# Optimization experiments

Measured on AMD Instinct MI355X. Metric: run time of the kernel, lower is better.

The kernel has to match this reference:

```python
import jax, jax.numpy as jnp
import numpy as np

N, E, G, T, H, ED, IN_D, OUT_D = 50000, 1600000, 64, 5, 64, 9, 10, 3
EPS = 1e-6

def _seg_mean(vals, seg, num):
    s = jax.ops.segment_sum(vals, seg, num_segments=num)
    c = jax.ops.segment_sum(jnp.ones((vals.shape[0],), vals.dtype), seg, num_segments=num)
    return s / jnp.maximum(c, 1.0)[:, None], c

def per_graph_edge_norm(edge_attr, edge_graph, num_graphs):
    # standardize each edge-feature column per graph (zero-shot transfer trick)
    mu, _ = _seg_mean(edge_attr, edge_graph, num_graphs)
    sq, _ = _seg_mean(edge_attr * edge_attr, edge_graph, num_graphs)
    var = jnp.maximum(sq - mu * mu, 0.0)
    std = jnp.sqrt(var)
    return (edge_attr - mu[edge_graph]) / (std[edge_graph] + EPS)

def setup_inputs() -> dict:
    key = jax.random.key(0)
    ks = jax.random.split(key, 24)
    s = 0.05  # weight scale to keep ReLU chains stable
    inp = {
        'x': jax.random.normal(ks[0], (N, IN_D), jnp.float32),
        'edge_index': jax.random.randint(ks[1], (2, E), 0, N),
        'edge_attr': jax.random.normal(ks[2], (E, ED), jnp.float32),
        'batch': jnp.sort(jax.random.randint(ks[3], (N,), 0, G)),
        'lift_W1': jax.random.normal(ks[4], (IN_D, H), jnp.float32) * s,
        'lift_b1': jnp.zeros((H,), jnp.float32),
        'lift_W2': jax.random.normal(ks[5], (H, H), jnp.float32) * s,
        'lift_b2': jnp.zeros((H,), jnp.float32),
        'Wself': jax.random.normal(ks[6], (T, H, H), jnp.float32) * s,
        'bself': jnp.zeros((T, H), jnp.float32),
        'msg_W0': jax.random.normal(ks[7], (T, H + ED, H), jnp.float32) * s,
        'msg_b0': jnp.zeros((T, H), jnp.float32),
        'msg_W1': jax.random.normal(ks[8], (T, H, H), jnp.float32) * s,
        'msg_b1': jnp.zeros((T, H), jnp.float32),
        'msg_W2': jax.random.normal(ks[9], (T, H, H), jnp.float32) * s,
        'msg_b2': jnp.zeros((T, H), jnp.float32),
        'gate_W': jax.random.normal(ks[10], (T, 1, H), jnp.float32) * s,
        'gate_b': jnp.zeros((T, H), jnp.float32),
        'proj_W1': jax.random.normal(ks[11], (H, H), jnp.float32) * s,
        'proj_b1': jnp.zeros((H,), jnp.float32),
        'proj_W2': jax.random.normal(ks[12], (H, OUT_D), jnp.float32) * s,
        'proj_b2': jnp.zeros((OUT_D,), jnp.float32),
    }
    return inp

def _gno(x, edge_index, edge_attr, batch,
         lift_W1, lift_b1, lift_W2, lift_b2,
         Wself, bself, msg_W0, msg_b0, msg_W1, msg_b1, msg_W2, msg_b2,
         gate_W, gate_b, proj_W1, proj_b1, proj_W2, proj_b2):
    src, dst = edge_index[0], edge_index[1]
    edge_graph = batch[src]
    ea = per_graph_edge_norm(edge_attr, edge_graph, G)  # cols 0:9 == all cols
    log_diag_y = x[:, 4:5]                               # [N,1]
    v0 = jax.nn.relu(x @ lift_W1 + lift_b1) @ lift_W2 + lift_b2  # lift
    v = v0
    for t in range(T):
        # gather -> per-edge MLP -> scatter-mean (AdmittanceKernelLayer)
        h = jnp.concatenate([v[src], ea], axis=-1)              # [E, H+ED]
        h = jax.nn.relu(h @ msg_W0[t] + msg_b0[t])
        h = jax.nn.relu(h @ msg_W1[t] + msg_b1[t])
        m = h @ msg_W2[t] + msg_b2[t]                           # [E, H]
        agg, _ = _seg_mean(m, dst, N)                           # mean aggregation
        gate = jax.nn.sigmoid(log_diag_y @ gate_W[t] + gate_b[t])  # [N,H]
        v = jax.nn.relu(v @ Wself[t] + bself[t] + agg + v0) * gate
        # dropout inactive at inference
    out = jax.nn.relu(v @ proj_W1 + proj_b1) @ proj_W2 + proj_b2  # project
    return out

def reference(x, edge_index, edge_attr, batch,
              lift_W1, lift_b1, lift_W2, lift_b2,
              Wself, bself, msg_W0, msg_b0, msg_W1, msg_b1, msg_W2, msg_b2,
              gate_W, gate_b, proj_W1, proj_b1, proj_W2, proj_b2):
    return _gno(x, edge_index, edge_attr, batch,
                lift_W1, lift_b1, lift_W2, lift_b2,
                Wself, bself, msg_W0, msg_b0, msg_W1, msg_b1, msg_W2, msg_b2,
                gate_W, gate_b, proj_W1, proj_b1, proj_W2, proj_b2)
```

## Files before the change

kernel.cpp:

```cpp
#include <hip/hip_runtime.h>
#include <math.h>

#define NN 50000
#define NE 1600000
#define NG 64
#define NT 5
#define NH 64
#define NED 9
#define NIN 10
#define NOUT 3
#define EPSF 1e-6f
#define NSUB (NE / 16)

typedef __attribute__((ext_vector_type(8))) short s8v;
typedef __attribute__((ext_vector_type(4))) short s4v;
typedef __attribute__((ext_vector_type(4))) float f32x4;

__device__ __forceinline__ unsigned short f2bf(float f) {
    union { float f; unsigned int u; } v; v.f = f;
    unsigned int r = v.u + 0x7FFFu + ((v.u >> 16) & 1u);
    return (unsigned short)(r >> 16);
}
__device__ __forceinline__ float bf2f(unsigned short b) {
    union { unsigned int u; float f; } v; v.u = ((unsigned int)b) << 16;
    return v.f;
}

__global__ void stats_kernel(const int* __restrict__ ei, const float* __restrict__ ea,
                             const int* __restrict__ batch,
                             float* __restrict__ ssum, float* __restrict__ ssq,
                             float* __restrict__ scnt, int* __restrict__ ecnt) {
    __shared__ float lsum[NG * NED];
    __shared__ float lsq[NG * NED];
    __shared__ float lcnt[NG];
    for (int i = threadIdx.x; i < NG * NED; i += blockDim.x) { lsum[i] = 0.f; lsq[i] = 0.f; }
    for (int i = threadIdx.x; i < NG; i += blockDim.x) lcnt[i] = 0.f;
    __syncthreads();
    int lane = threadIdx.x & 63;
    int stride = gridDim.x * blockDim.x;
    for (int e = blockIdx.x * blockDim.x + threadIdx.x; e < NE; e += stride) {
        int s = ei[e];
        int g = batch[s];
        atomicAdd(&ecnt[ei[NE + e]], 1);
        float a[NED];
#pragma unroll
        for (int d = 0; d < NED; ++d) a[d] = ea[(size_t)e * NED + d];
        int g0 = __builtin_amdgcn_readfirstlane(g);
        if (__all(g == g0)) {
            float sv[NED], qv[NED];
#pragma unroll
            for (int d = 0; d < NED; ++d) { sv[d] = a[d]; qv[d] = a[d] * a[d]; }
#pragma unroll
            for (int off = 32; off; off >>= 1) {
#pragma unroll
                for (int d = 0; d < NED; ++d) {
                    sv[d] += __shfl_down(sv[d], off);
                    qv[d] += __shfl_down(qv[d], off);
                }
            }
            if (lane == 0) {
#pragma unroll
                for (int d = 0; d < NED; ++d) {
                    atomicAdd(&lsum[g0 * NED + d], sv[d]);
                    atomicAdd(&lsq[g0 * NED + d], qv[d]);
                }
                atomicAdd(&lcnt[g0], 64.f);
            }
        } else {
            atomicAdd(&lcnt[g], 1.0f);
#pragma unroll
            for (int d = 0; d < NED; ++d) {
                atomicAdd(&lsum[g * NED + d], a[d]);
                atomicAdd(&lsq[g * NED + d], a[d] * a[d]);
            }
        }
    }
    __syncthreads();
    for (int i = threadIdx.x; i < NG * NED; i += blockDim.x) {
        atomicAdd(&ssum[i], lsum[i]);
        atomicAdd(&ssq[i], lsq[i]);
    }
    for (int i = threadIdx.x; i < NG; i += blockDim.x) atomicAdd(&scnt[i], lcnt[i]);
}

__global__ void stats_fin(const float* __restrict__ ssum, const float* __restrict__ ssq,
                          const float* __restrict__ scnt,
                          float* __restrict__ mu, float* __restrict__ rstd) {
    int i = blockIdx.x * blockDim.x + threadIdx.x;
    if (i >= NG * NED) return;
    int g = i / NED;
    float c = fmaxf(scnt[g], 1.0f);
    float m = ssum[i] / c;
    float q = ssq[i] / c;
    float var = fmaxf(q - m * m, 0.f);
    mu[i] = m;
    rstd[i] = 1.0f / (sqrtf(var) + EPSF);
}

__global__ void scan1_kernel(const int* __restrict__ ecnt, int* __restrict__ partial) {
    __shared__ int sm[256];
    int i = blockIdx.x * 256 + threadIdx.x;
    sm[threadIdx.x] = (i < NN) ? ecnt[i] : 0;
    __syncthreads();
    for (int off = 128; off; off >>= 1) {
        if (threadIdx.x < off) sm[threadIdx.x] += sm[threadIdx.x + off];
        __syncthreads();
    }
    if (threadIdx.x == 0) partial[blockIdx.x] = sm[0];
}
__global__ void scan2_kernel(int* __restrict__ partial, int nb) {
    __shared__ int sm[256];
    int t = threadIdx.x;
    sm[t] = (t < nb) ? partial[t] : 0;
    __syncthreads();
    for (int off = 1; off < 256; off <<= 1) {
        int v = (t >= off) ? sm[t - off] : 0;
        __syncthreads();
        sm[t] += v;
        __syncthreads();
    }
    if (t < nb) partial[t] = (t ? sm[t - 1] : 0);
}
__global__ void scan3_kernel(const int* __restrict__ ecnt, const int* __restrict__ partial,
                             int* __restrict__ offs) {
    __shared__ int sm[256];
    int b = blockIdx.x, t = threadIdx.x, i = b * 256 + t;
    int x = (i < NN) ? ecnt[i] : 0;
    sm[t] = x;
    __syncthreads();
    for (int off = 1; off < 256; off <<= 1) {
        int v = (t >= off) ? sm[t - off] : 0;
        __syncthreads();
        sm[t] += v;
        __syncthreads();
    }
    if (i < NN) offs[i] = sm[t] - x + partial[b];
}

__global__ void permute_kernel(const int* __restrict__ ei, const int* __restrict__ offs,
                               int* __restrict__ cursor, int* __restrict__ perm) {
    int stride = gridDim.x * blockDim.x;
    for (int e = blockIdx.x * blockDim.x + threadIdx.x; e < NE; e += stride) {
        int d = ei[NE + e];
        int pos = offs[d] + atomicAdd(&cursor[d], 1);
        perm[pos] = e;
    }
}

__global__ void pack_kernel(const int* __restrict__ perm, const int* __restrict__ ei,
                            const float* __restrict__ ea, const int* __restrict__ batch,
                            const float* __restrict__ mu, const float* __restrict__ rstd,
                            int* __restrict__ srcPerm, int* __restrict__ dstPerm,
                            unsigned short* __restrict__ eaN) {
    int stride = gridDim.x * blockDim.x;
    for (int p = blockIdx.x * blockDim.x + threadIdx.x; p < NE; p += stride) {
        int e = perm[p];
        int s = ei[e], d = ei[NE + e];
        int g = batch[s];
        srcPerm[p] = s;
        dstPerm[p] = d;
#pragma unroll
        for (int k = 0; k < NED; ++k) {
            float val = (ea[(size_t)e * NED + k] - mu[g * NED + k]) * rstd[g * NED + k];
            eaN[(size_t)k * NE + p] = f2bf(val);
        }
    }
}

__global__ __launch_bounds__(256) void lift_kernel(
    const float* __restrict__ x,
    const float* __restrict__ W1, const float* __restrict__ b1,
    const float* __restrict__ W2, const float* __restrict__ b2,
    float* __restrict__ v0, float* __restrict__ v, float* __restrict__ ldy) {
    __shared__ float sW1[NIN * NH];
    __shared__ __align__(16) float sW2[NH][NH];
    __shared__ float sb1[NH], sb2[NH];
    for (int i = threadIdx.x; i < NIN * NH; i += blockDim.x) sW1[i] = W1[i];
    for (int i = threadIdx.x; i < NH * NH; i += blockDim.x) {
        int k = i >> 6, j = i & 63;
        sW2[j][k] = W2[i];
    }
    for (int i = threadIdx.x; i < NH; i += blockDim.x) { sb1[i] = b1[i]; sb2[i] = b2[i]; }
    __syncthreads();
    int stride = gridDim.x * blockDim.x;
    for (int n = blockIdx.x * blockDim.x + threadIdx.x; n < NN; n += stride) {
        float xr[NIN];
#pragma unroll
        for (int k = 0; k < NIN; ++k) xr[k] = x[(size_t)n * NIN + k];
        ldy[n] = xr[4];
        float h[NH];
#pragma unroll
        for (int j = 0; j < NH; ++j) {
            float acc = sb1[j];
#pragma unroll
            for (int k = 0; k < NIN; ++k) acc += xr[k] * sW1[k * NH + j];
            h[j] = fmaxf(acc, 0.f);
        }
#pragma unroll
        for (int j = 0; j < NH; ++j) {
            float acc = sb2[j];
#pragma unroll
            for (int k = 0; k < NH; k += 4) {
                float4 w = *(const float4*)&sW2[j][k];
                acc += h[k] * w.x + h[k + 1] * w.y + h[k + 2] * w.z + h[k + 3] * w.w;
            }
            v0[(size_t)n * NH + j] = acc;
            v[(size_t)n * NH + j] = acc;
        }
    }
}

__device__ __forceinline__ void gemm_acc68(const float* __restrict__ Ab,
                                           const float* __restrict__ Wb,
                                           int K, int te, int tj, float acc[4][4]) {
#pragma unroll 4
    for (int k = 0; k < K; ++k) {
        float4 a = *(const float4*)(Ab + k * 68 + (te << 2));
        float4 b = *(const float4*)(Wb + (k << 6) + (tj << 2));
        acc[0][0] = fmaf(a.x, b.x, acc[0][0]);
        acc[0][1] = fmaf(a.x, b.y, acc[0][1]);
        acc[0][2] = fmaf(a.x, b.z, acc[0][2]);
        acc[0][3] = fmaf(a.x, b.w, acc[0][3]);
        acc[1][0] = fmaf(a.y, b.x, acc[1][0]);
        acc[1][1] = fmaf(a.y, b.y, acc[1][1]);
        acc[1][2] = fmaf(a.y, b.z, acc[1][2]);
        acc[1][3] = fmaf(a.y, b.w, acc[1][3]);
        acc[2][0] = fmaf(a.z, b.x, acc[2][0]);
        acc[2][1] = fmaf(a.z, b.y, acc[2][1]);
        acc[2][2] = fmaf(a.z, b.z, acc[2][2]);
        acc[2][3] = fmaf(a.z, b.w, acc[2][3]);
        acc[3][0] = fmaf(a.w, b.x, acc[3][0]);
        acc[3][1] = fmaf(a.w, b.y, acc[3][1]);
        acc[3][2] = fmaf(a.w, b.z, acc[3][2]);
        acc[3][3] = fmaf(a.w, b.w, acc[3][3]);
    }
}

__global__ __launch_bounds__(256, 4) void u_kernel(
    const float* __restrict__ v, const float* __restrict__ W0v,
    const float* __restrict__ b0, float* __restrict__ U) {
    __shared__ __align__(16) float Vt[64][68];
    __shared__ __align__(16) float sW[64][64];
    __shared__ float sb[64];
    const int tid = threadIdx.x;
    const int base = blockIdx.x * 64;
    const int te = tid >> 4, tj = tid & 15;

    {
        int r = tid >> 2;
        int kb = (tid & 3) << 4;
        int n = base + r;
        const float4* vrow = (const float4*)(v + (size_t)n * NH + kb);
#pragma unroll
        for (int q = 0; q < 4; ++q) {
            float4 f = (n < NN) ? vrow[q] : make_float4(0.f, 0.f, 0.f, 0.f);
            int k = kb + q * 4;
            Vt[k + 0][r] = f.x; Vt[k + 1][r] = f.y; Vt[k + 2][r] = f.z; Vt[k + 3][r] = f.w;
        }
    }
    for (int i4 = tid; i4 < 64 * 16; i4 += 256) {
        int k = i4 >> 4, c4 = i4 & 15;
        *(float4*)&sW[k][c4 * 4] = *(const float4*)(W0v + (size_t)k * 64 + c4 * 4);
    }
    if (tid < 64) sb[tid] = b0[tid];
    __syncthreads();

    float acc[4][4];
    {
        float b0_ = sb[tj * 4 + 0], b1_ = sb[tj * 4 + 1], b2_ = sb[tj * 4 + 2], b3_ = sb[tj * 4 + 3];
#pragma unroll
        for (int ee = 0; ee < 4; ++ee) { acc[ee][0] = b0_; acc[ee][1] = b1_; acc[ee][2] = b2_; acc[ee][3] = b3_; }
    }
    gemm_acc68(&Vt[0][0], &sW[0][0], 64, te, tj, acc);

#pragma unroll
    for (int ee = 0; ee < 4; ++ee) {
        int n = base + te * 4 + ee;
        if (n < NN)
            *(float4*)&U[(size_t)n * NH + tj * 4] =
                make_float4(acc[ee][0], acc[ee][1], acc[ee][2], acc[ee][3]);
    }
}

__global__ __launch_bounds__(256, 4) void edge4_kernel(
    const int* __restrict__ srcPerm, const int* __restrict__ dstPerm,
    const unsigned short* __restrict__ eaN,
    const float* __restrict__ W0e, const float* __restrict__ W1, const float* __restrict__ b1,
    const float* __restrict__ U, float* __restrict__ nodesum) {
    __shared__ __align__(16) float sWe[NED][64];
    __shared__ __align__(16) short W1frag[8][64][8];
    __shared__ __align__(16) short h0bf[4][16 * 64];
    __shared__ __align__(16) float h1s[4][16 * 64];
    __shared__ int sDstS[4][16];

    const int tid = threadIdx.x;
    const int lane = tid & 63, w = tid >> 6;
    const int l15 = lane & 15, l4 = lane >> 4;

    for (int i4 = tid; i4 < NED * 16; i4 += 256) {
        int k = i4 >> 4, c4 = i4 & 15;
        *(float4*)&sWe[k][c4 * 4] = *(const float4*)(W0e + (size_t)k * 64 + c4 * 4);
    }
    for (int idx = tid; idx < 2 * 4 * 64; idx += 256) {
        int kc = idx >> 8, c = (idx >> 6) & 3, ln = idx & 63;
        int fl15 = ln & 15, fl4 = ln >> 4;
        int col = 16 * c + fl15;
        s8v frag;
#pragma unroll
        for (int j = 0; j < 8; ++j) {
            int k = kc * 32 + fl4 * 8 + j;
            frag[j] = (short)f2bf(W1[(size_t)k * 64 + col]);
        }
        *(s8v*)&W1frag[kc * 4 + c][ln][0] = frag;
    }
    float b1r[4];
#pragma unroll
    for (int c = 0; c < 4; ++c) b1r[c] = b1[16 * c + l15];
    __syncthreads();

    short* myh0 = h0bf[w];
    float* myh1 = h1s[w];
    int*   myd  = sDstS[w];
    const int gw = blockIdx.x * 4 + w;
    const int nw = gridDim.x * 4;

    for (int st = gw; st < NSUB; st += nw) {
        const int e16 = st * 16;
        if (lane < 16) myd[lane] = dstPerm[e16 + lane];

        int4 s4 = *(const int4*)(srcPerm + e16 + 4 * l4);
        ushort4 eu[NED];
#pragma unroll
        for (int d = 0; d < NED; ++d)
            eu[d] = *(const ushort4*)(eaN + (size_t)d * NE + e16 + 4 * l4);

        float acc0[4][4];
        {
            const int* sp = (const int*)&s4;
#pragma unroll
            for (int ee = 0; ee < 4; ++ee) {
                float4 u4 = *(const float4*)(U + (size_t)sp[ee] * NH + 4 * l15);
                acc0[ee][0] = u4.x; acc0[ee][1] = u4.y; acc0[ee][2] = u4.z; acc0[ee][3] = u4.w;
            }
        }
#pragma unroll
        for (int d = 0; d < NED; ++d) {
            float4 wv = *(const float4*)&sWe[d][4 * l15];
            float a0 = bf2f(eu[d].x), a1 = bf2f(eu[d].y), a2 = bf2f(eu[d].z), a3 = bf2f(eu[d].w);
            acc0[0][0] = fmaf(a0, wv.x, acc0[0][0]); acc0[0][1] = fmaf(a0, wv.y, acc0[0][1]);
            acc0[0][2] = fmaf(a0, wv.z, acc0[0][2]); acc0[0][3] = fmaf(a0, wv.w, acc0[0][3]);
            acc0[1][0] = fmaf(a1, wv.x, acc0[1][0]); acc0[1][1] = fmaf(a1, wv.y, acc0[1][1]);
            acc0[1][2] = fmaf(a1, wv.z, acc0[1][2]); acc0[1][3] = fmaf(a1, wv.w, acc0[1][3]);
            acc0[2][0] = fmaf(a2, wv.x, acc0[2][0]); acc0[2][1] = fmaf(a2, wv.y, acc0[2][1]);
            acc0[2][2] = fmaf(a2, wv.z, acc0[2][2]); acc0[2][3] = fmaf(a2, wv.w, acc0[2][3]);
            acc0[3][0] = fmaf(a3, wv.x, acc0[3][0]); acc0[3][1] = fmaf(a3, wv.y, acc0[3][1]);
            acc0[3][2] = fmaf(a3, wv.z, acc0[3][2]); acc0[3][3] = fmaf(a3, wv.w, acc0[3][3]);
        }

#pragma unroll
        for (int ee = 0; ee < 4; ++ee) {
            int row = 4 * l4 + ee;
            s4v p;
            p[0] = (short)f2bf(fmaxf(acc0[ee][0], 0.f));
            p[1] = (short)f2bf(fmaxf(acc0[ee][1], 0.f));
            p[2] = (short)f2bf(fmaxf(acc0[ee][2], 0.f));
            p[3] = (short)f2bf(fmaxf(acc0[ee][3], 0.f));
            *(s4v*)((char*)myh0 + row * 128 + ((l15 * 8) ^ ((row & 7) << 4))) = p;
        }

        f32x4 acc[4];
#pragma unroll
        for (int c = 0; c < 4; ++c) {
            float b = b1r[c];
            acc[c][0] = b; acc[c][1] = b; acc[c][2] = b; acc[c][3] = b;
        }
        {
            const char* abase = (const char*)myh0 + l15 * 128;
            const int aswz = (l15 & 7) << 4;
#pragma unroll
            for (int kc = 0; kc < 2; ++kc) {
                s8v af = *(const s8v*)(abase + ((l4 * 16 + kc * 64) ^ aswz));
#pragma unroll
                for (int c = 0; c < 4; ++c) {
                    s8v bf = *(const s8v*)&W1frag[kc * 4 + c][lane][0];
                    acc[c] = __builtin_amdgcn_mfma_f32_16x16x32_bf16(af, bf, acc[c], 0, 0, 0);
                }
            }
        }

        int dFirst = myd[0];
        int dLast = myd[15];
        if (dFirst == dLast) {
#pragma unroll
            for (int c = 0; c < 4; ++c) {
                float vs = fmaxf(acc[c][0], 0.f) + fmaxf(acc[c][1], 0.f) +
                           fmaxf(acc[c][2], 0.f) + fmaxf(acc[c][3], 0.f);
                vs += __shfl_xor(vs, 16);
                vs += __shfl_xor(vs, 32);
                if (l4 == 0)
                    atomicAdd(&nodesum[(size_t)dFirst * NH + 16 * c + l15], vs);
            }
        } else {
#pragma unroll
            for (int r = 0; r < 4; ++r) {
                int row = 4 * l4 + r;
#pragma unroll
                for (int c = 0; c < 4; ++c)
                    myh1[row * 64 + ((16 * c + l15) ^ (l4 * 8))] = fmaxf(acc[c][r], 0.f);
            }
            int cur = dFirst;
            float a = myh1[lane];
#pragma unroll
            for (int i = 1; i < 16; ++i) {
                int dn = myd[i];
                float hv = myh1[i * 64 + (lane ^ ((i >> 2) * 8))];
                if (dn != cur) {
                    atomicAdd(&nodesum[(size_t)cur * NH + lane], a);
                    cur = dn;
                    a = hv;
                } else {
                    a += hv;
                }
            }
            atomicAdd(&nodesum[(size_t)cur * NH + lane], a);
        }
    }
}

__global__ __launch_bounds__(256, 2) void update3_kernel(
    const float* __restrict__ Wself, const float* __restrict__ bself,
    const float* __restrict__ W2, const float* __restrict__ b2,
    const float* __restrict__ gWt, const float* __restrict__ gbt,
    const float* __restrict__ v0, const float* __restrict__ ldy,
    const int* __restrict__ ecnt, const float* __restrict__ nodesum,
    float* __restrict__ v) {
    __shared__ __align__(16) float Vt[64][68];
    __shared__ __align__(16) float St[64][68];
    __shared__ __align__(16) float sWs[64][64];
    __shared__ __align__(16) float sW2[64][64];
    __shared__ float sbs[64], sb2[64], sgw[64], sgb[64];
    const int tid = threadIdx.x;
    const int base = blockIdx.x * 64;
    const int te = tid >> 4, tj = tid & 15;

    {
        int r = tid >> 2;
        int kb = (tid & 3) << 4;
        int n = base + r;
        const float4* vrow = (const float4*)(v + (size_t)n * NH + kb);
        const float4* srow = (const float4*)(nodesum + (size_t)n * NH + kb);
#pragma unroll
        for (int q = 0; q < 4; ++q) {
            float4 f = (n < NN) ? vrow[q] : make_float4(0.f, 0.f, 0.f, 0.f);
            float4 g = (n < NN) ? srow[q] : make_float4(0.f, 0.f, 0.f, 0.f);
            int k = kb + q * 4;
            Vt[k + 0][r] = f.x; Vt[k + 1][r] = f.y; Vt[k + 2][r] = f.z; Vt[k + 3][r] = f.w;
            St[k + 0][r] = g.x; St[k + 1][r] = g.y; St[k + 2][r] = g.z; St[k + 3][r] = g.w;
        }
    }
    for (int i4 = tid; i4 < 64 * 16; i4 += 256) {
        int k = i4 >> 4, c4 = i4 & 15;
        *(float4*)&sWs[k][c4 * 4] = *(const float4*)(Wself + (size_t)k * 64 + c4 * 4);
        *(float4*)&sW2[k][c4 * 4] = *(const float4*)(W2 + (size_t)k * 64 + c4 * 4);
    }
    if (tid < 64) { sbs[tid] = bself[tid]; sb2[tid] = b2[tid]; sgw[tid] = gWt[tid]; sgb[tid] = gbt[tid]; }
    __syncthreads();

    float acc1[4][4], acc2[4][4];
    {
        float b0_ = sbs[tj * 4 + 0], b1_ = sbs[tj * 4 + 1], b2_ = sbs[tj * 4 + 2], b3_ = sbs[tj * 4 + 3];
#pragma unroll
        for (int ee = 0; ee < 4; ++ee) {
            acc1[ee][0] = b0_; acc1[ee][1] = b1_; acc1[ee][2] = b2_; acc1[ee][3] = b3_;
            acc2[ee][0] = 0.f; acc2[ee][1] = 0.f; acc2[ee][2] = 0.f; acc2[ee][3] = 0.f;
        }
    }
    gemm_acc68(&Vt[0][0], &sWs[0][0], 64, te, tj, acc1);
    gemm_acc68(&St[0][0], &sW2[0][0], 64, te, tj, acc2);

    float gw0 = sgw[tj * 4 + 0], gw1 = sgw[tj * 4 + 1], gw2 = sgw[tj * 4 + 2], gw3 = sgw[tj * 4 + 3];
    float gb0 = sgb[tj * 4 + 0], gb1 = sgb[tj * 4 + 1], gb2 = sgb[tj * 4 + 2], gb3 = sgb[tj * 4 + 3];
    float bb0 = sb2[tj * 4 + 0], bb1 = sb2[tj * 4 + 1], bb2 = sb2[tj * 4 + 2], bb3 = sb2[tj * 4 + 3];
#pragma unroll
    for (int ee = 0; ee < 4; ++ee) {
        int n = base + te * 4 + ee;
        if (n >= NN) continue;
        float cnt = (float)ecnt[n];
        float has = (cnt > 0.5f) ? 1.f : 0.f;
        float dninv = has / fmaxf(cnt, 1.f);
        float ld = ldy[n];
        float4 v0r = *(const float4*)&v0[(size_t)n * NH + tj * 4];
        float z0 = acc1[ee][0] + acc2[ee][0] * dninv + bb0 * has + v0r.x;
        float z1 = acc1[ee][1] + acc2[ee][1] * dninv + bb1 * has + v0r.y;
        float z2 = acc1[ee][2] + acc2[ee][2] * dninv + bb2 * has + v0r.z;
        float z3 = acc1[ee][3] + acc2[ee][3] * dninv + bb3 * has + v0r.w;
        float g0 = 1.f / (1.f + expf(-(ld * gw0 + gb0)));
        float g1 = 1.f / (1.f + expf(-(ld * gw1 + gb1)));
        float g2 = 1.f / (1.f + expf(-(ld * gw2 + gb2)));
        float g3 = 1.f / (1.f + expf(-(ld * gw3 + gb3)));
        *(float4*)&v[(size_t)n * NH + tj * 4] =
            make_float4(fmaxf(z0, 0.f) * g0, fmaxf(z1, 0.f) * g1,
                        fmaxf(z2, 0.f) * g2, fmaxf(z3, 0.f) * g3);
    }
}

__global__ __launch_bounds__(256) void proj_kernel(
    const float* __restrict__ v,
    const float* __restrict__ pW1, const float* __restrict__ pb1,
    const float* __restrict__ pW2, const float* __restrict__ pb2,
    float* __restrict__ out) {
    __shared__ __align__(16) float sW1[NH][NH];
    __shared__ float sb1[NH];
    __shared__ float sW2[NH * NOUT];
    __shared__ float sb2[NOUT];
    for (int i = threadIdx.x; i < NH * NH; i += blockDim.x) {
        int k = i >> 6, j = i & 63;
        sW1[j][k] = pW1[i];
    }
    for (int i = threadIdx.x; i < NH; i += blockDim.x) sb1[i] = pb1[i];
    for (int i = threadIdx.x; i < NH * NOUT; i += blockDim.x) sW2[i] = pW2[i];
    for (int i = threadIdx.x; i < NOUT; i += blockDim.x) sb2[i] = pb2[i];
    __syncthreads();
    int stride = gridDim.x * blockDim.x;
    for (int n = blockIdx.x * blockDim.x + threadIdx.x; n < NN; n += stride) {
        float vr[NH];
        const float4* vp = (const float4*)(v + (size_t)n * NH);
#pragma unroll
        for (int q = 0; q < NH / 4; ++q) {
            float4 f = vp[q];
            vr[4 * q + 0] = f.x; vr[4 * q + 1] = f.y; vr[4 * q + 2] = f.z; vr[4 * q + 3] = f.w;
        }
        float o0 = sb2[0], o1 = sb2[1], o2 = sb2[2];
#pragma unroll
        for (int j = 0; j < NH; ++j) {
            float acc = sb1[j];
#pragma unroll
            for (int k = 0; k < NH; k += 4) {
                float4 w = *(const float4*)&sW1[j][k];
                acc += vr[k] * w.x + vr[k + 1] * w.y + vr[k + 2] * w.z + vr[k + 3] * w.w;
            }
            float h = fmaxf(acc, 0.f);
            o0 += h * sW2[j * NOUT + 0];
            o1 += h * sW2[j * NOUT + 1];
            o2 += h * sW2[j * NOUT + 2];
        }
        out[(size_t)n * NOUT + 0] = o0;
        out[(size_t)n * NOUT + 1] = o1;
        out[(size_t)n * NOUT + 2] = o2;
    }
}

extern "C" void kernel_launch(void* const* d_in, const int* in_sizes, int n_in,
                              void* d_out, int out_size, void* d_ws, size_t ws_size,
                              hipStream_t stream) {
    (void)in_sizes; (void)n_in; (void)out_size; (void)ws_size;
    const float* x     = (const float*)d_in[0];
    const int*   ei    = (const int*)d_in[1];
    const float* ea    = (const float*)d_in[2];
    const int*   batch = (const int*)d_in[3];
    const float* lW1   = (const float*)d_in[4];
    const float* lb1   = (const float*)d_in[5];
    const float* lW2   = (const float*)d_in[6];
    const float* lb2   = (const float*)d_in[7];
    const float* Wself = (const float*)d_in[8];
    const float* bself = (const float*)d_in[9];
    const float* mW0   = (const float*)d_in[10];
    const float* mb0   = (const float*)d_in[11];
    const float* mW1   = (const float*)d_in[12];
    const float* mb1   = (const float*)d_in[13];
    const float* mW2   = (const float*)d_in[14];
    const float* mb2   = (const float*)d_in[15];
    const float* gW    = (const float*)d_in[16];
    const float* gb    = (const float*)d_in[17];
    const float* pW1   = (const float*)d_in[18];
    const float* pb1   = (const float*)d_in[19];
    const float* pW2   = (const float*)d_in[20];
    const float* pb2   = (const float*)d_in[21];
    float* out = (float*)d_out;
    float* ws  = (float*)d_ws;

    float* nodesum = ws;
    float* v0   = nodesum + (size_t)NN * NH;
    float* v    = v0 + (size_t)NN * NH;
    float* U    = v + (size_t)NN * NH;
    float* ldy  = U + (size_t)NN * NH;
    float* mu   = ldy + NN;
    float* rstd = mu + NG * NED;
    float* ssum = rstd + NG * NED;
    float* ssq  = ssum + NG * NED;
    float* scnt = ssq + NG * NED;
    int*   ecnt   = (int*)(scnt + NG);
    int*   cursor = ecnt + NN;
    int*   offs    = cursor + NN;
    int*   partial = offs + NN;
    int*   srcPerm = partial + 256;
    int*   dstPerm = srcPerm + NE;
    unsigned short* eaN = (unsigned short*)(dstPerm + NE);
    int*   perm = (int*)nodesum;

    const int NBLK = (NN + 63) / 64;
    const int SBLK = (NN + 255) / 256;

    hipMemsetAsync(ssum, 0, ((size_t)(2 * NG * NED + NG) + 2 * NN) * sizeof(float), stream);

    stats_kernel<<<512, 256, 0, stream>>>(ei, ea, batch, ssum, ssq, scnt, ecnt);
    stats_fin<<<3, 256, 0, stream>>>(ssum, ssq, scnt, mu, rstd);
    scan1_kernel<<<SBLK, 256, 0, stream>>>(ecnt, partial);
    scan2_kernel<<<1, 256, 0, stream>>>(partial, SBLK);
    scan3_kernel<<<SBLK, 256, 0, stream>>>(ecnt, partial, offs);
    permute_kernel<<<2048, 256, 0, stream>>>(ei, offs, cursor, perm);
    pack_kernel<<<2048, 256, 0, stream>>>(perm, ei, ea, batch, mu, rstd, srcPerm, dstPerm, eaN);
    lift_kernel<<<200, 256, 0, stream>>>(x, lW1, lb1, lW2, lb2, v0, v, ldy);

    for (int t = 0; t < NT; ++t) {
        const float* W0t = mW0 + (size_t)t * (NH + NED) * NH;
        hipMemsetAsync(nodesum, 0, (size_t)NN * NH * sizeof(float), stream);
        u_kernel<<<NBLK, 256, 0, stream>>>(v, W0t, mb0 + (size_t)t * NH, U);
        edge4_kernel<<<1024, 256, 0, stream>>>(
            srcPerm, dstPerm, eaN,
            W0t + (size_t)NH * NH,
            mW1 + (size_t)t * NH * NH, mb1 + (size_t)t * NH,
            U, nodesum);
        update3_kernel<<<NBLK, 256, 0, stream>>>(
            Wself + (size_t)t * NH * NH, bself + (size_t)t * NH,
            mW2 + (size_t)t * NH * NH, mb2 + (size_t)t * NH,
            gW + (size_t)t * NH, gb + (size_t)t * NH,
            v0, ldy, ecnt, nodesum, v);
    }
    proj_kernel<<<200, 256, 0, stream>>>(v, pW1, pb1, pW2, pb2, out);
}
```

Baseline: 1.366 ms.

## Replace global stats atomics with per-block partials and fold nodesum zeroing into update

The stats kernel now writes each block's shared-memory partial sums to a private slice, and a separate merge kernel reduces them deterministically, removing global float atomics and the wavefront-uniform shuffle fast path. The update kernel zeroes nodesum after reading it, so the per-iteration memset is replaced by a single memset before the loop. This saves four full 12.8MB memsets, at the cost of an extra store per element in update, a serial 1024-iteration merge loop, and simpler per-lane LDS atomics in stats.

Result: slower. 1.432 ms (+4.8%).

```diff
diff --git a/kernel.cpp b/kernel.cpp
--- a/kernel.cpp
+++ b/kernel.cpp
@@ -11,6 +11,8 @@
 #define NOUT 3
 #define EPSF 1e-6f
 #define NSUB (NE / 16)
+#define STATS_BLKS 1024
+#define STATS_SLICE (2 * NG * NED + NG)
 
 typedef __attribute__((ext_vector_type(8))) short s8v;
 typedef __attribute__((ext_vector_type(4))) short s4v;
@@ -26,61 +28,48 @@
     return v.f;
 }
 
-__global__ void stats_kernel(const int* __restrict__ ei, const float* __restrict__ ea,
-                             const int* __restrict__ batch,
-                             float* __restrict__ ssum, float* __restrict__ ssq,
-                             float* __restrict__ scnt, int* __restrict__ ecnt) {
+__global__ __launch_bounds__(256) void stats_kernel(
+    const int* __restrict__ ei, const float* __restrict__ ea,
+    const int* __restrict__ batch,
+    float* __restrict__ blockAcc, int* __restrict__ ecnt) {
     __shared__ float lsum[NG * NED];
     __shared__ float lsq[NG * NED];
     __shared__ float lcnt[NG];
     for (int i = threadIdx.x; i < NG * NED; i += blockDim.x) { lsum[i] = 0.f; lsq[i] = 0.f; }
     for (int i = threadIdx.x; i < NG; i += blockDim.x) lcnt[i] = 0.f;
     __syncthreads();
-    int lane = threadIdx.x & 63;
     int stride = gridDim.x * blockDim.x;
     for (int e = blockIdx.x * blockDim.x + threadIdx.x; e < NE; e += stride) {
         int s = ei[e];
         int g = batch[s];
         atomicAdd(&ecnt[ei[NE + e]], 1);
-        float a[NED];
-#pragma unroll
-        for (int d = 0; d < NED; ++d) a[d] = ea[(size_t)e * NED + d];
-        int g0 = __builtin_amdgcn_readfirstlane(g);
-        if (__all(g == g0)) {
-            float sv[NED], qv[NED];
-#pragma unroll
-            for (int d = 0; d < NED; ++d) { sv[d] = a[d]; qv[d] = a[d] * a[d]; }
-#pragma unroll
-            for (int off = 32; off; off >>= 1) {
-#pragma unroll
-                for (int d = 0; d < NED; ++d) {
-                    sv[d] += __shfl_down(sv[d], off);
-                    qv[d] += __shfl_down(qv[d], off);
-                }
-            }
-            if (lane == 0) {
-#pragma unroll
-                for (int d = 0; d < NED; ++d) {
-                    atomicAdd(&lsum[g0 * NED + d], sv[d]);
-                    atomicAdd(&lsq[g0 * NED + d], qv[d]);
-                }
-                atomicAdd(&lcnt[g0], 64.f);
-            }
-        } else {
-            atomicAdd(&lcnt[g], 1.0f);
-#pragma unroll
-            for (int d = 0; d < NED; ++d) {
-                atomicAdd(&lsum[g * NED + d], a[d]);
-                atomicAdd(&lsq[g * NED + d], a[d] * a[d]);
-            }
-        }
-    }
-    __syncthreads();
+        atomicAdd(&lcnt[g], 1.0f);
+#pragma unroll
+        for (int d = 0; d < NED; ++d) {
+            float a = ea[(size_t)e * NED + d];
+            atomicAdd(&lsum[g * NED + d], a);
+            atomicAdd(&lsq[g * NED + d], a * a);
+        }
+    }
+    __syncthreads();
+    float* dst = blockAcc + (size_t)blockIdx.x * STATS_SLICE;
     for (int i = threadIdx.x; i < NG * NED; i += blockDim.x) {
-        atomicAdd(&ssum[i], lsum[i]);
-        atomicAdd(&ssq[i], lsq[i]);
-    }
-    for (int i = threadIdx.x; i < NG; i += blockDim.x) atomicAdd(&scnt[i], lcnt[i]);
+        dst[i] = lsum[i];
+        dst[NG * NED + i] = lsq[i];
+    }
+    for (int i = threadIdx.x; i < NG; i += blockDim.x) dst[2 * NG * NED + i] = lcnt[i];
+}
+
+__global__ void stats_merge(const float* __restrict__ blockAcc,
+                            float* __restrict__ ssum, float* __restrict__ ssq,
+                            float* __restrict__ scnt) {
+    int i = blockIdx.x * 256 + threadIdx.x;
+    if (i >= STATS_SLICE) return;
+    float a = 0.f;
+    for (int b = 0; b < STATS_BLKS; ++b) a += blockAcc[(size_t)b * STATS_SLICE + i];
+    if (i < NG * NED) ssum[i] = a;
+    else if (i < 2 * NG * NED) ssq[i - NG * NED] = a;
+    else scnt[i - 2 * NG * NED] = a;
 }
 
 __global__ void stats_fin(const float* __restrict__ ssum, const float* __restrict__ ssq,
@@ -346,7 +335,8 @@
 #pragma unroll
         for (int d = 0; d < NED; ++d) {
             float4 wv = *(const float4*)&sWe[d][4 * l15];
-            float a0 = bf2f(eu[d].x), a1 = bf2f(eu[d].y), a2 = bf2f(eu[d].z), a3 = bf2f(eu[d].w);
+            float a0 = bf2f((unsigned short)eu[d].x), a1 = bf2f((unsigned short)eu[d].y);
+            float a2 = bf2f((unsigned short)eu[d].z), a3 = bf2f((unsigned short)eu[d].w);
             acc0[0][0] = fmaf(a0, wv.x, acc0[0][0]); acc0[0][1] = fmaf(a0, wv.y, acc0[0][1]);
             acc0[0][2] = fmaf(a0, wv.z, acc0[0][2]); acc0[0][3] = fmaf(a0, wv.w, acc0[0][3]);
             acc0[1][0] = fmaf(a1, wv.x, acc0[1][0]); acc0[1][1] = fmaf(a1, wv.y, acc0[1][1]);
@@ -432,7 +422,7 @@
     const float* __restrict__ W2, const float* __restrict__ b2,
     const float* __restrict__ gWt, const float* __restrict__ gbt,
     const float* __restrict__ v0, const float* __restrict__ ldy,
-    const int* __restrict__ ecnt, const float* __restrict__ nodesum,
+    const int* __restrict__ ecnt, float* __restrict__ nodesum,
     float* __restrict__ v) {
     __shared__ __align__(16) float Vt[64][68];
     __shared__ __align__(16) float St[64][68];
@@ -448,11 +438,13 @@
         int kb = (tid & 3) << 4;
         int n = base + r;
         const float4* vrow = (const float4*)(v + (size_t)n * NH + kb);
-        const float4* srow = (const float4*)(nodesum + (size_t)n * NH + kb);
+        float4* srow = (float4*)(nodesum + (size_t)n * NH + kb);
+        const float4 z4 = make_float4(0.f, 0.f, 0.f, 0.f);
 #pragma unroll
         for (int q = 0; q < 4; ++q) {
-            float4 f = (n < NN) ? vrow[q] : make_float4(0.f, 0.f, 0.f, 0.f);
-            float4 g = (n < NN) ? srow[q] : make_float4(0.f, 0.f, 0.f, 0.f);
+            float4 f = (n < NN) ? vrow[q] : z4;
+            float4 g = (n < NN) ? srow[q] : z4;
+            if (n < NN) srow[q] = z4;
             int k = kb + q * 4;
             Vt[k + 0][r] = f.x; Vt[k + 1][r] = f.y; Vt[k + 2][r] = f.z; Vt[k + 3][r] = f.w;
             St[k + 0][r] = g.x; St[k + 1][r] = g.y; St[k + 2][r] = g.z; St[k + 3][r] = g.w;
@@ -596,14 +588,16 @@
     int*   srcPerm = partial + 256;
     int*   dstPerm = srcPerm + NE;
     unsigned short* eaN = (unsigned short*)(dstPerm + NE);
+    float* statsPart = (float*)(eaN + (size_t)NED * NE);
     int*   perm = (int*)nodesum;
 
     const int NBLK = (NN + 63) / 64;
     const int SBLK = (NN + 255) / 256;
 
-    hipMemsetAsync(ssum, 0, ((size_t)(2 * NG * NED + NG) + 2 * NN) * sizeof(float), stream);
-
-    stats_kernel<<<512, 256, 0, stream>>>(ei, ea, batch, ssum, ssq, scnt, ecnt);
+    hipMemsetAsync(ecnt, 0, (size_t)2 * NN * sizeof(int), stream);
+
+    stats_kernel<<<STATS_BLKS, 256, 0, stream>>>(ei, ea, batch, statsPart, ecnt);
+    stats_merge<<<(STATS_SLICE + 255) / 256, 256, 0, stream>>>(statsPart, ssum, ssq, scnt);
     stats_fin<<<3, 256, 0, stream>>>(ssum, ssq, scnt, mu, rstd);
     scan1_kernel<<<SBLK, 256, 0, stream>>>(ecnt, partial);
     scan2_kernel<<<1, 256, 0, stream>>>(partial, SBLK);
@@ -612,9 +606,10 @@
     pack_kernel<<<2048, 256, 0, stream>>>(perm, ei, ea, batch, mu, rstd, srcPerm, dstPerm, eaN);
     lift_kernel<<<200, 256, 0, stream>>>(x, lW1, lb1, lW2, lb2, v0, v, ldy);
 
+    hipMemsetAsync(nodesum, 0, (size_t)NN * NH * sizeof(float), stream);
+
     for (int t = 0; t < NT; ++t) {
         const float* W0t = mW0 + (size_t)t * (NH + NED) * NH;
-        hipMemsetAsync(nodesum, 0, (size_t)NN * NH * sizeof(float), stream);
         u_kernel<<<NBLK, 256, 0, stream>>>(v, W0t, mb0 + (size_t)t * NH, U);
         edge4_kernel<<<1024, 256, 0, stream>>>(
             srcPerm, dstPerm, eaN,
```
